# Performance work log

Hardware: AMD Instinct MI355X
Metric: run time of the kernel (lower is better)

The kernel has to match this reference:

```python
import jax, jax.numpy as jnp
import numpy as np

N_NODES = 100000
N_EDGES = 1600000
NUM_FEATURES = 128
HIDDEN = 64
NUM_CLASSES = 16


def setup_inputs() -> dict:
    key = jax.random.key(0)
    k1, k2, k3, k4 = jax.random.split(key, 4)
    x = jax.random.normal(k1, (N_NODES, NUM_FEATURES), dtype=jnp.float32)
    edge_index = jax.random.randint(k2, (2, N_EDGES), 0, N_NODES, dtype=jnp.int64)
    # Glorot-ish scaled weights ([in, out] layout; PyG stores [out,in] but math is x @ W)
    W1 = jax.random.normal(k3, (NUM_FEATURES, HIDDEN), dtype=jnp.float32) * (1.0 / np.sqrt(NUM_FEATURES))
    W2 = jax.random.normal(k4, (HIDDEN, NUM_CLASSES), dtype=jnp.float32) * (1.0 / np.sqrt(HIDDEN))
    return {"x": x, "edge_index": edge_index, "W1": W1, "W2": W2}


def _gcn_conv(x, edge_index, W):
    # GCNConv(add_self_loops=False, bias=False): linear then sym-normalized scatter-add.
    n = x.shape[0]
    row, col = edge_index[0], edge_index[1]  # source -> target
    h = x @ W  # [N, out]
    # degree from unit edge weights scattered on target nodes
    deg = jax.ops.segment_sum(jnp.ones(row.shape[0], dtype=h.dtype), col, num_segments=n)
    deg_inv_sqrt = jnp.where(deg > 0, jax.lax.rsqrt(jnp.maximum(deg, 1.0)), 0.0)
    norm = deg_inv_sqrt[row] * deg_inv_sqrt[col]  # [E]
    msg = h[row] * norm[:, None]  # gather + scale, [E, out]
    return jax.ops.segment_sum(msg, col, num_segments=n)  # scatter-add to targets


def reference(x, edge_index, W1, W2):
    h = _gcn_conv(x, edge_index, W1)
    h = _gcn_conv(h, edge_index, W2)
    return jax.nn.log_softmax(h, axis=1)
```

## Files before the change

### kernel.cpp

```cpp
#include <hip/hip_runtime.h>
#include <hip/hip_bf16.h>
#include <hip/hip_fp16.h>


#define STRIDE 48
#define BCAP   6144


__global__ __launch_bounds__(256) void k_bucket(const int* __restrict__ ei,
                                                const void* __restrict__ xv,
                                                const void* __restrict__ W1v,
                                                const void* __restrict__ W2v,
                                                int* __restrict__ flags,
                                                float* __restrict__ W12,
                                                int* __restrict__ bcnt,
                                                int* __restrict__ buf,
                                                int e, int n, int nb) {
    __shared__ int hist[512];
    __shared__ int basec[512];
    __shared__ float wtmp[2048];
    __shared__ int sraw, sbad;
    int t = threadIdx.x;
    int b = blockIdx.x;

    if (t == 0) { sraw = 0; sbad = 0; }
    for (int i = t; i < nb; i += 256) hist[i] = 0;
    __syncthreads();

    {
        int i = b * 4096 + t;
        if (i < e && ei[2 * (size_t)i + 1] != 0) atomicOr(&sraw, 1);
    }
    if (b < 8) {
        const unsigned short* xs = (const unsigned short*)xv;
        int bad = 0;
        for (int i = t; i < 1024; i += 256) {
            unsigned ex2 = (xs[i] >> 7) & 0xFF;
            if (ex2 >= 0x90) bad = 1;
        }
        if (bad) atomicOr(&sbad, 1);
    }
    __syncthreads();
    int raw = sraw ? 0 : 1;

    if (b < 8) {
        bool f32 = sbad != 0;
        if (f32) {
            const float* W1 = (const float*)W1v;
            const float* W2 = (const float*)W2v;
            for (int i = t; i < 1024; i += 256) {
                wtmp[i] = W1[b * 1024 + i];
                wtmp[1024 + i] = W2[i];
            }
        } else {
            const __hip_bfloat16* W1 = (const __hip_bfloat16*)W1v;
            const __hip_bfloat16* W2 = (const __hip_bfloat16*)W2v;
            for (int i = t; i < 1024; i += 256) {
                wtmp[i] = __bfloat162float(W1[b * 1024 + i]);
                wtmp[1024 + i] = __bfloat162float(W2[i]);
            }
        }
    }

    int e0 = b * 4096;
    int bk[16], rec[16];
#pragma unroll
    for (int j = 0; j < 16; ++j) {
        int i = e0 + j * 256 + t;
        bk[j] = -1;
        if (i < e) {
            int r, c;
            if (raw) {
                r = ((const int2*)ei)[(size_t)i].x;
                c = ((const int2*)ei)[(size_t)e + i].x;
            } else {
                r = ei[i];
                c = ei[(size_t)e + i];
            }
            if ((unsigned)c < (unsigned)n && (unsigned)r < (unsigned)n) {
                bk[j] = c >> 8;
                rec[j] = ((c & 255) << 17) | r;
                atomicAdd(&hist[bk[j]], 1);
            }
        }
    }
    __syncthreads();

    if (b < 8) {
        int kl = t >> 4, c = t & 15;
        float acc = 0.0f;
#pragma unroll 8
        for (int f = 0; f < 64; ++f) acc += wtmp[kl * 64 + f] * wtmp[1024 + f * 16 + c];
        W12[(16 * b + kl) * 16 + c] = acc;
        if (b == 0 && t == 0) { flags[0] = sbad; flags[1] = raw; }
    }

    for (int i = t; i < nb; i += 256) {
        int h = hist[i];
        basec[i] = h ? atomicAdd(&bcnt[i], h) : 0;
    }
    __syncthreads();
#pragma unroll
    for (int j = 0; j < 16; ++j) {
        if (bk[j] >= 0) {
            int slot = atomicAdd(&basec[bk[j]], 1);
            if (slot < BCAP) buf[(size_t)bk[j] * BCAP + slot] = rec[j];
        }
    }
}


__global__ __launch_bounds__(256) void k_csr_z(const int* __restrict__ bcnt,
                                               const int* __restrict__ buf,
                                               const void* __restrict__ xv,
                                               const float* __restrict__ W12,
                                               const int* __restrict__ flags,
                                               int* __restrict__ cnt,
                                               int* __restrict__ csr,
                                               __half* __restrict__ z, int n) {
    __shared__ int lcnt[256];
    __shared__ int lcsr[256 * STRIDE];
    int t = threadIdx.x;
    int b = blockIdx.x;
    lcnt[t] = 0;
    int4 zero4 = {0, 0, 0, 0};
    for (int i = t; i < 256 * STRIDE / 4; i += 256) ((int4*)lcsr)[i] = zero4;
    __syncthreads();

    int node = (b << 8) + t;
    bool f32 = flags[0] != 0;

    uint4 xpre[16];
    bool pre = (!f32) && (node < n);
    if (pre) {
        const uint4* x4 = (const uint4*)xv + (size_t)node * 16;
#pragma unroll
        for (int j = 0; j < 16; ++j) xpre[j] = x4[j];
    }

    int m = bcnt[b];
    if (m > BCAP) m = BCAP;
    for (int i = t; i < m; i += 256) {
        int rec = buf[(size_t)b * BCAP + i];
        int cl = rec >> 17;
        int r = rec & 0x1FFFF;
        int slot = atomicAdd(&lcnt[cl], 1);
        if (slot < STRIDE) lcsr[cl * STRIDE + slot] = r;
    }
    __syncthreads();
    int deg = lcnt[t];
    if (node < n) cnt[node] = deg;
    const int4* src = (const int4*)lcsr;
    int4* dst = (int4*)csr + (size_t)b * (256 * STRIDE / 4);
    for (int i = t; i < 256 * STRIDE / 4; i += 256) dst[i] = src[i];

    if (node >= n) return;
    float acc[16];
#pragma unroll
    for (int c = 0; c < 16; ++c) acc[c] = 0.0f;

    if (f32) {
        const float4* x4 = (const float4*)xv + (size_t)node * 32;
        for (int j = 0; j < 16; ++j) {
            float4 v0 = x4[2 * j];
            float4 v1 = x4[2 * j + 1];
            float xk[8] = {v0.x, v0.y, v0.z, v0.w, v1.x, v1.y, v1.z, v1.w};
#pragma unroll
            for (int k8 = 0; k8 < 8; ++k8) {
                const float* w = &W12[(8 * j + k8) * 16];
                float xx = xk[k8];
#pragma unroll
                for (int c = 0; c < 16; ++c) acc[c] += xx * w[c];
            }
        }
    } else {
#pragma unroll
        for (int j = 0; j < 16; ++j) {
            uint4 v = xpre[j];
            float xk[8];
            xk[0] = __uint_as_float(v.x << 16);
            xk[1] = __uint_as_float(v.x & 0xffff0000u);
            xk[2] = __uint_as_float(v.y << 16);
            xk[3] = __uint_as_float(v.y & 0xffff0000u);
            xk[4] = __uint_as_float(v.z << 16);
            xk[5] = __uint_as_float(v.z & 0xffff0000u);
            xk[6] = __uint_as_float(v.w << 16);
            xk[7] = __uint_as_float(v.w & 0xffff0000u);
#pragma unroll
            for (int k8 = 0; k8 < 8; ++k8) {
                const float* w = &W12[(8 * j + k8) * 16];
                float xx = xk[k8];
#pragma unroll
                for (int c = 0; c < 16; ++c) acc[c] += xx * w[c];
            }
        }
    }

    float di = (deg > 0) ? rsqrtf((float)deg) : 0.0f;
    __half2 hh[8];
#pragma unroll
    for (int c2 = 0; c2 < 8; ++c2)
        hh[c2] = __halves2half2(__float2half(acc[2 * c2] * di),
                                __float2half(acc[2 * c2 + 1] * di));
    uint4* zdst = (uint4*)(z + (size_t)node * 16);
    uint4 u0, u1;
    u0.x = *(unsigned*)&hh[0]; u0.y = *(unsigned*)&hh[1];
    u0.z = *(unsigned*)&hh[2]; u0.w = *(unsigned*)&hh[3];
    u1.x = *(unsigned*)&hh[4]; u1.y = *(unsigned*)&hh[5];
    u1.z = *(unsigned*)&hh[6]; u1.w = *(unsigned*)&hh[7];
    zdst[0] = u0;
    zdst[1] = u1;
}


__global__ __launch_bounds__(256) void k_agg1b(const int* __restrict__ cnt,
                                               const int* __restrict__ csr,
                                               const __half* __restrict__ z,
                                               __half* __restrict__ z2, int n) {
    int t = threadIdx.x;
    int wid = t >> 6, lane = t & 63;
    int half = lane >> 5, l5 = lane & 31;
    int node0 = blockIdx.x * 8 + wid * 2 + half;
    int node = node0 < n ? node0 : n - 1;
    int id = csr[(size_t)node * STRIDE + l5];
    int deg = cnt[node];
    float di = (deg > 0) ? rsqrtf((float)deg) : 0.0f;
    int m = deg < STRIDE ? deg : STRIDE;
    int sub = l5 >> 3, f2 = l5 & 7;
    int base = half << 5;
    const __half2* zp = (const __half2*)z;
    float ax = 0.0f, ay = 0.0f;
#pragma unroll
    for (int j = 0; j < 16; j += 4) {
        int s = __shfl(id, base + j + sub);
        float2 v = __half22float2(zp[(size_t)s * 8 + f2]);
        bool ok = (j + sub) < m;
        ax += ok ? v.x : 0.0f;
        ay += ok ? v.y : 0.0f;
    }
    if (__any(m > 16)) {
#pragma unroll
        for (int j = 16; j < 24; j += 4) {
            int s = __shfl(id, base + j + sub);
            float2 v = __half22float2(zp[(size_t)s * 8 + f2]);
            bool ok = (j + sub) < m;
            ax += ok ? v.x : 0.0f;
            ay += ok ? v.y : 0.0f;
        }
        if (__any(m > 24)) {
#pragma unroll
            for (int j = 24; j < 32; j += 4) {
                int s = __shfl(id, base + j + sub);
                float2 v = __half22float2(zp[(size_t)s * 8 + f2]);
                bool ok = (j + sub) < m;
                ax += ok ? v.x : 0.0f;
                ay += ok ? v.y : 0.0f;
            }
            if (__any(m > 32)) {
                int id2 = csr[(size_t)node * STRIDE + 32 + (l5 & 15)];
                for (int j = 32; j < 48; j += 4) {
                    int s = __shfl(id2, base + (j - 32) + sub);
                    if (j + sub < m) {
                        float2 v = __half22float2(zp[(size_t)s * 8 + f2]);
                        ax += v.x;
                        ay += v.y;
                    }
                }
            }
        }
    }
    ax += __shfl_xor(ax, 8);  ay += __shfl_xor(ay, 8);
    ax += __shfl_xor(ax, 16); ay += __shfl_xor(ay, 16);
    float s2 = di * di;
    if (node0 < n && l5 < 8)
        ((__half2*)z2)[(size_t)node * 8 + l5] =
            __halves2half2(__float2half(ax * s2), __float2half(ay * s2));
}


__global__ __launch_bounds__(256) void k_agg2b(const int* __restrict__ cnt,
                                               const int* __restrict__ csr,
                                               const __half* __restrict__ z2,
                                               const int* __restrict__ flags,
                                               void* __restrict__ outv, int n) {
    int t = threadIdx.x;
    int wid = t >> 6, lane = t & 63;
    int half = lane >> 5, l5 = lane & 31;
    int node0 = blockIdx.x * 8 + wid * 2 + half;
    int node = node0 < n ? node0 : n - 1;
    int id = csr[(size_t)node * STRIDE + l5];
    int deg = cnt[node];
    float di = (deg > 0) ? rsqrtf((float)deg) : 0.0f;
    int m = deg < STRIDE ? deg : STRIDE;
    int sub = l5 >> 3, f2 = l5 & 7;
    int base = half << 5;
    const __half2* zp = (const __half2*)z2;
    float ax = 0.0f, ay = 0.0f;
#pragma unroll
    for (int j = 0; j < 16; j += 4) {
        int s = __shfl(id, base + j + sub);
        float2 v = __half22float2(zp[(size_t)s * 8 + f2]);
        bool ok = (j + sub) < m;
        ax += ok ? v.x : 0.0f;
        ay += ok ? v.y : 0.0f;
    }
    if (__any(m > 16)) {
#pragma unroll
        for (int j = 16; j < 24; j += 4) {
            int s = __shfl(id, base + j + sub);
            float2 v = __half22float2(zp[(size_t)s * 8 + f2]);
            bool ok = (j + sub) < m;
            ax += ok ? v.x : 0.0f;
            ay += ok ? v.y : 0.0f;
        }
        if (__any(m > 24)) {
#pragma unroll
            for (int j = 24; j < 32; j += 4) {
                int s = __shfl(id, base + j + sub);
                float2 v = __half22float2(zp[(size_t)s * 8 + f2]);
                bool ok = (j + sub) < m;
                ax += ok ? v.x : 0.0f;
                ay += ok ? v.y : 0.0f;
            }
            if (__any(m > 32)) {
                int id2 = csr[(size_t)node * STRIDE + 32 + (l5 & 15)];
                for (int j = 32; j < 48; j += 4) {
                    int s = __shfl(id2, base + (j - 32) + sub);
                    if (j + sub < m) {
                        float2 v = __half22float2(zp[(size_t)s * 8 + f2]);
                        ax += v.x;
                        ay += v.y;
                    }
                }
            }
        }
    }
    ax += __shfl_xor(ax, 8);  ay += __shfl_xor(ay, 8);
    ax += __shfl_xor(ax, 16); ay += __shfl_xor(ay, 16);
    float vx = ax * di, vy = ay * di;
    float mx = fmaxf(vx, vy);
#pragma unroll
    for (int d = 1; d <= 4; d <<= 1) mx = fmaxf(mx, __shfl_xor(mx, d));
    float es = __expf(vx - mx) + __expf(vy - mx);
#pragma unroll
    for (int d = 1; d <= 4; d <<= 1) es += __shfl_xor(es, d);
    float ls = __logf(es);
    float rx = vx - mx - ls, ry = vy - mx - ls;
    if (node0 < n && l5 < 8) {
        if (flags[0]) {
            float2 r; r.x = rx; r.y = ry;
            ((float2*)outv)[(size_t)node * 8 + l5] = r;
        } else {
            __hip_bfloat162 hh;
            hh.x = __float2bfloat16(rx);
            hh.y = __float2bfloat16(ry);
            ((__hip_bfloat162*)outv)[(size_t)node * 8 + l5] = hh;
        }
    }
}


extern "C" void kernel_launch(void* const* d_in, const int* in_sizes, int n_in,
                              void* d_out, int out_size, void* d_ws, size_t ws_size,
                              hipStream_t stream) {
    const int F = 128, C = 16;
    int n = in_sizes[0] / F;
    int e = in_sizes[1] / 2;
    int nb = (n + 255) >> 8;

    const void* x = d_in[0];
    const int* ei = (const int*)d_in[1];
    const void* W1 = d_in[2];
    const void* W2 = d_in[3];

    char* p = (char*)d_ws;
    auto carve = [&](size_t bytes) {
        char* r = p;
        p += (bytes + 255) & ~(size_t)255;
        return r;
    };
    int*    flags = (int*)  carve(256);
    int*    bcnt  = (int*)  carve((size_t)nb * 4);
    int*    cnt   = (int*)  carve((size_t)n * 4);
    float*  W12   = (float*)carve(128 * 16 * 4);
    int*    csr   = (int*)  carve(((size_t)nb * 256 * STRIDE + 64) * 4);
    __half* z     = (__half*)carve((size_t)n * C * 2);
    size_t buf_sz = (size_t)nb * BCAP * 4;
    size_t z2_sz = (size_t)n * C * 2;
    char* regionB = carve(buf_sz > z2_sz ? buf_sz : z2_sz);
    int*    buf = (int*)regionB;
    __half* z2  = (__half*)regionB;
    (void)ws_size;

    int gb_bucket = (e + 4095) / 4096;
    if (gb_bucket < 8) gb_bucket = 8;

    hipMemsetAsync(bcnt, 0, (size_t)nb * 4, stream);
    k_bucket<<<gb_bucket, 256, 0, stream>>>(ei, x, W1, W2, flags, W12, bcnt, buf, e, n, nb);
    k_csr_z<<<nb, 256, 0, stream>>>(bcnt, buf, x, W12, flags, cnt, csr, z, n);
    k_agg1b<<<(n + 7) / 8, 256, 0, stream>>>(cnt, csr, z, z2, n);
    k_agg2b<<<(n + 7) / 8, 256, 0, stream>>>(cnt, csr, z2, flags, d_out, n);
}
```

Before: 171.1 us.

## Split CSR build and projection into separate kernels with 4-node register blocking

Splits the fused CSR-build-plus-projection kernel in two. The new k_csr only builds the CSR in shared memory. The new k_z computes x·W12 with 64-thread blocks, where each thread handles 4 nodes so every weight load is reused four times, and it reads degrees back from global memory. This is meant to free the projection from the large shared-memory footprint of the CSR build, which limited occupancy. The trade-off is an extra launch, a degree round-trip through global memory, and uncoalesced strided x loads. The aggregation kernels also make the first 24 neighbours unconditional instead of 16, cutting one wave-uniform branch level.

```diff
diff --git a/kernel.cpp b/kernel.cpp
--- a/kernel.cpp
+++ b/kernel.cpp
@@ -110,14 +110,10 @@
 }
 
 
-__global__ __launch_bounds__(256) void k_csr_z(const int* __restrict__ bcnt,
-                                               const int* __restrict__ buf,
-                                               const void* __restrict__ xv,
-                                               const float* __restrict__ W12,
-                                               const int* __restrict__ flags,
-                                               int* __restrict__ cnt,
-                                               int* __restrict__ csr,
-                                               __half* __restrict__ z, int n) {
+__global__ __launch_bounds__(256) void k_csr(const int* __restrict__ bcnt,
+                                             const int* __restrict__ buf,
+                                             int* __restrict__ cnt,
+                                             int* __restrict__ csr, int n) {
     __shared__ int lcnt[256];
     __shared__ int lcsr[256 * STRIDE];
     int t = threadIdx.x;
@@ -126,17 +122,6 @@
     int4 zero4 = {0, 0, 0, 0};
     for (int i = t; i < 256 * STRIDE / 4; i += 256) ((int4*)lcsr)[i] = zero4;
     __syncthreads();
-
-    int node = (b << 8) + t;
-    bool f32 = flags[0] != 0;
-
-    uint4 xpre[16];
-    bool pre = (!f32) && (node < n);
-    if (pre) {
-        const uint4* x4 = (const uint4*)xv + (size_t)node * 16;
-#pragma unroll
-        for (int j = 0; j < 16; ++j) xpre[j] = x4[j];
-    }
 
     int m = bcnt[b];
     if (m > BCAP) m = BCAP;
@@ -148,68 +133,115 @@
         if (slot < STRIDE) lcsr[cl * STRIDE + slot] = r;
     }
     __syncthreads();
-    int deg = lcnt[t];
-    if (node < n) cnt[node] = deg;
+    int node = (b << 8) + t;
+    if (node < n) cnt[node] = lcnt[t];
     const int4* src = (const int4*)lcsr;
     int4* dst = (int4*)csr + (size_t)b * (256 * STRIDE / 4);
     for (int i = t; i < 256 * STRIDE / 4; i += 256) dst[i] = src[i];
-
-    if (node >= n) return;
-    float acc[16];
-#pragma unroll
-    for (int c = 0; c < 16; ++c) acc[c] = 0.0f;
+}
+
+
+__global__ __launch_bounds__(64) void k_z(const void* __restrict__ xv,
+                                          const float* __restrict__ W12,
+                                          const int* __restrict__ flags,
+                                          const int* __restrict__ cnt,
+                                          __half* __restrict__ z, int n) {
+    int t = threadIdx.x;
+    int base = blockIdx.x * 256 + t;
+    bool f32 = flags[0] != 0;
+
+    float acc[4][16];
+#pragma unroll
+    for (int a = 0; a < 4; ++a)
+#pragma unroll
+        for (int c = 0; c < 16; ++c) acc[a][c] = 0.0f;
 
     if (f32) {
-        const float4* x4 = (const float4*)xv + (size_t)node * 32;
+        const float4* x4 = (const float4*)xv;
         for (int j = 0; j < 16; ++j) {
-            float4 v0 = x4[2 * j];
-            float4 v1 = x4[2 * j + 1];
-            float xk[8] = {v0.x, v0.y, v0.z, v0.w, v1.x, v1.y, v1.z, v1.w};
+            float xk[4][8];
+#pragma unroll
+            for (int a = 0; a < 4; ++a) {
+                int node = base + 64 * a;
+                if (node < n) {
+                    float4 v0 = x4[(size_t)node * 32 + 2 * j];
+                    float4 v1 = x4[(size_t)node * 32 + 2 * j + 1];
+                    xk[a][0] = v0.x; xk[a][1] = v0.y; xk[a][2] = v0.z; xk[a][3] = v0.w;
+                    xk[a][4] = v1.x; xk[a][5] = v1.y; xk[a][6] = v1.z; xk[a][7] = v1.w;
+                } else {
+#pragma unroll
+                    for (int q = 0; q < 8; ++q) xk[a][q] = 0.0f;
+                }
+            }
 #pragma unroll
             for (int k8 = 0; k8 < 8; ++k8) {
                 const float* w = &W12[(8 * j + k8) * 16];
-                float xx = xk[k8];
-#pragma unroll
-                for (int c = 0; c < 16; ++c) acc[c] += xx * w[c];
+#pragma unroll
+                for (int c = 0; c < 16; ++c) {
+                    float wc = w[c];
+                    acc[0][c] += xk[0][k8] * wc;
+                    acc[1][c] += xk[1][k8] * wc;
+                    acc[2][c] += xk[2][k8] * wc;
+                    acc[3][c] += xk[3][k8] * wc;
+                }
             }
         }
     } else {
-#pragma unroll
+        const uint4* x4 = (const uint4*)xv;
         for (int j = 0; j < 16; ++j) {
-            uint4 v = xpre[j];
-            float xk[8];
-            xk[0] = __uint_as_float(v.x << 16);
-            xk[1] = __uint_as_float(v.x & 0xffff0000u);
-            xk[2] = __uint_as_float(v.y << 16);
-            xk[3] = __uint_as_float(v.y & 0xffff0000u);
-            xk[4] = __uint_as_float(v.z << 16);
-            xk[5] = __uint_as_float(v.z & 0xffff0000u);
-            xk[6] = __uint_as_float(v.w << 16);
-            xk[7] = __uint_as_float(v.w & 0xffff0000u);
+            uint4 v[4];
+#pragma unroll
+            for (int a = 0; a < 4; ++a) {
+                int node = base + 64 * a;
+                v[a] = (node < n) ? x4[(size_t)node * 16 + j] : uint4{0u, 0u, 0u, 0u};
+            }
 #pragma unroll
             for (int k8 = 0; k8 < 8; ++k8) {
                 const float* w = &W12[(8 * j + k8) * 16];
-                float xx = xk[k8];
-#pragma unroll
-                for (int c = 0; c < 16; ++c) acc[c] += xx * w[c];
-            }
-        }
-    }
-
-    float di = (deg > 0) ? rsqrtf((float)deg) : 0.0f;
-    __half2 hh[8];
-#pragma unroll
-    for (int c2 = 0; c2 < 8; ++c2)
-        hh[c2] = __halves2half2(__float2half(acc[2 * c2] * di),
-                                __float2half(acc[2 * c2 + 1] * di));
-    uint4* zdst = (uint4*)(z + (size_t)node * 16);
-    uint4 u0, u1;
-    u0.x = *(unsigned*)&hh[0]; u0.y = *(unsigned*)&hh[1];
-    u0.z = *(unsigned*)&hh[2]; u0.w = *(unsigned*)&hh[3];
-    u1.x = *(unsigned*)&hh[4]; u1.y = *(unsigned*)&hh[5];
-    u1.z = *(unsigned*)&hh[6]; u1.w = *(unsigned*)&hh[7];
-    zdst[0] = u0;
-    zdst[1] = u1;
+                unsigned word[4];
+#pragma unroll
+                for (int a = 0; a < 4; ++a) {
+                    unsigned uw = (k8 < 2) ? v[a].x : (k8 < 4) ? v[a].y
+                                : (k8 < 6) ? v[a].z : v[a].w;
+                    word[a] = (k8 & 1) ? (uw & 0xffff0000u) : (uw << 16);
+                }
+                float xa = __uint_as_float(word[0]);
+                float xb = __uint_as_float(word[1]);
+                float xc = __uint_as_float(word[2]);
+                float xd = __uint_as_float(word[3]);
+#pragma unroll
+                for (int c = 0; c < 16; ++c) {
+                    float wc = w[c];
+                    acc[0][c] += xa * wc;
+                    acc[1][c] += xb * wc;
+                    acc[2][c] += xc * wc;
+                    acc[3][c] += xd * wc;
+                }
+            }
+        }
+    }
+
+#pragma unroll
+    for (int a = 0; a < 4; ++a) {
+        int node = base + 64 * a;
+        if (node < n) {
+            int d = cnt[node];
+            float di = (d > 0) ? rsqrtf((float)d) : 0.0f;
+            __half2 hh[8];
+#pragma unroll
+            for (int c2 = 0; c2 < 8; ++c2)
+                hh[c2] = __halves2half2(__float2half(acc[a][2 * c2] * di),
+                                        __float2half(acc[a][2 * c2 + 1] * di));
+            uint4* zdst = (uint4*)(z + (size_t)node * 16);
+            uint4 u0, u1;
+            u0.x = *(unsigned*)&hh[0]; u0.y = *(unsigned*)&hh[1];
+            u0.z = *(unsigned*)&hh[2]; u0.w = *(unsigned*)&hh[3];
+            u1.x = *(unsigned*)&hh[4]; u1.y = *(unsigned*)&hh[5];
+            u1.z = *(unsigned*)&hh[6]; u1.w = *(unsigned*)&hh[7];
+            zdst[0] = u0;
+            zdst[1] = u1;
+        }
+    }
 }
 
 
@@ -231,40 +263,30 @@
     const __half2* zp = (const __half2*)z;
     float ax = 0.0f, ay = 0.0f;
 #pragma unroll
-    for (int j = 0; j < 16; j += 4) {
+    for (int j = 0; j < 24; j += 4) {
         int s = __shfl(id, base + j + sub);
         float2 v = __half22float2(zp[(size_t)s * 8 + f2]);
         bool ok = (j + sub) < m;
         ax += ok ? v.x : 0.0f;
         ay += ok ? v.y : 0.0f;
     }
-    if (__any(m > 16)) {
-#pragma unroll
-        for (int j = 16; j < 24; j += 4) {
+    if (__any(m > 24)) {
+#pragma unroll
+        for (int j = 24; j < 32; j += 4) {
             int s = __shfl(id, base + j + sub);
             float2 v = __half22float2(zp[(size_t)s * 8 + f2]);
             bool ok = (j + sub) < m;
             ax += ok ? v.x : 0.0f;
             ay += ok ? v.y : 0.0f;
         }
-        if (__any(m > 24)) {
-#pragma unroll
-            for (int j = 24; j < 32; j += 4) {
-                int s = __shfl(id, base + j + sub);
-                float2 v = __half22float2(zp[(size_t)s * 8 + f2]);
-                bool ok = (j + sub) < m;
-                ax += ok ? v.x : 0.0f;
-                ay += ok ? v.y : 0.0f;
-            }
-            if (__any(m > 32)) {
-                int id2 = csr[(size_t)node * STRIDE + 32 + (l5 & 15)];
-                for (int j = 32; j < 48; j += 4) {
-                    int s = __shfl(id2, base + (j - 32) + sub);
-                    if (j + sub < m) {
-                        float2 v = __half22float2(zp[(size_t)s * 8 + f2]);
-                        ax += v.x;
-                        ay += v.y;
-                    }
+        if (__any(m > 32)) {
+            int id2 = csr[(size_t)node * STRIDE + 32 + (l5 & 15)];
+            for (int j = 32; j < 48; j += 4) {
+                int s = __shfl(id2, base + (j - 32) + sub);
+                if (j + sub < m) {
+                    float2 v = __half22float2(zp[(size_t)s * 8 + f2]);
+                    ax += v.x;
+                    ay += v.y;
                 }
             }
         }
@@ -297,40 +319,30 @@
     const __half2* zp = (const __half2*)z2;
     float ax = 0.0f, ay = 0.0f;
 #pragma unroll
-    for (int j = 0; j < 16; j += 4) {
+    for (int j = 0; j < 24; j += 4) {
         int s = __shfl(id, base + j + sub);
         float2 v = __half22float2(zp[(size_t)s * 8 + f2]);
         bool ok = (j + sub) < m;
         ax += ok ? v.x : 0.0f;
         ay += ok ? v.y : 0.0f;
     }
-    if (__any(m > 16)) {
-#pragma unroll
-        for (int j = 16; j < 24; j += 4) {
+    if (__any(m > 24)) {
+#pragma unroll
+        for (int j = 24; j < 32; j += 4) {
             int s = __shfl(id, base + j + sub);
             float2 v = __half22float2(zp[(size_t)s * 8 + f2]);
             bool ok = (j + sub) < m;
             ax += ok ? v.x : 0.0f;
             ay += ok ? v.y : 0.0f;
         }
-        if (__any(m > 24)) {
-#pragma unroll
-            for (int j = 24; j < 32; j += 4) {
-                int s = __shfl(id, base + j + sub);
-                float2 v = __half22float2(zp[(size_t)s * 8 + f2]);
-                bool ok = (j + sub) < m;
-                ax += ok ? v.x : 0.0f;
-                ay += ok ? v.y : 0.0f;
-            }
-            if (__any(m > 32)) {
-                int id2 = csr[(size_t)node * STRIDE + 32 + (l5 & 15)];
-                for (int j = 32; j < 48; j += 4) {
-                    int s = __shfl(id2, base + (j - 32) + sub);
-                    if (j + sub < m) {
-                        float2 v = __half22float2(zp[(size_t)s * 8 + f2]);
-                        ax += v.x;
-                        ay += v.y;
-                    }
+        if (__any(m > 32)) {
+            int id2 = csr[(size_t)node * STRIDE + 32 + (l5 & 15)];
+            for (int j = 32; j < 48; j += 4) {
+                int s = __shfl(id2, base + (j - 32) + sub);
+                if (j + sub < m) {
+                    float2 v = __half22float2(zp[(size_t)s * 8 + f2]);
+                    ax += v.x;
+                    ay += v.y;
                 }
             }
         }
@@ -397,7 +409,8 @@
 
     hipMemsetAsync(bcnt, 0, (size_t)nb * 4, stream);
     k_bucket<<<gb_bucket, 256, 0, stream>>>(ei, x, W1, W2, flags, W12, bcnt, buf, e, n, nb);
-    k_csr_z<<<nb, 256, 0, stream>>>(bcnt, buf, x, W12, flags, cnt, csr, z, n);
+    k_csr<<<nb, 256, 0, stream>>>(bcnt, buf, cnt, csr, n);
+    k_z<<<(n + 255) / 256, 64, 0, stream>>>(x, W12, flags, cnt, z, n);
     k_agg1b<<<(n + 7) / 8, 256, 0, stream>>>(cnt, csr, z, z2, n);
     k_agg2b<<<(n + 7) / 8, 256, 0, stream>>>(cnt, csr, z2, flags, d_out, n);
 }
```

Result: slower. 190.7 us (+11.5%).
